# Performance work log

Hardware: AMD Instinct MI355X
Metric: run time of the kernel (lower is better)

## Reference

```python
import jax, jax.numpy as jnp
from jax import lax
import numpy as np

CODE_DIM = 256
CODE_SIZE = 1024
BETA = 0.25


def _conv2d(x, w, b, stride, pad):
    # x: NCHW, w: OIHW (pytorch Conv2d layout)
    y = lax.conv_general_dilated(x, w, (stride, stride), [(pad, pad), (pad, pad)],
                                 dimension_numbers=('NCHW', 'OIHW', 'NCHW'))
    return y + b[None, :, None, None]


def _conv_transpose2d(x, w, b, stride, pad):
    # w: pytorch ConvTranspose2d layout [in, out, kh, kw]
    kh, kw = w.shape[2], w.shape[3]
    wf = jnp.flip(w, (2, 3)).transpose(1, 0, 2, 3)  # -> OIHW with spatial flip
    y = lax.conv_general_dilated(x, wf, (1, 1),
                                 [(kh - 1 - pad, kh - 1 - pad), (kw - 1 - pad, kw - 1 - pad)],
                                 lhs_dilation=(stride, stride),
                                 dimension_numbers=('NCHW', 'OIHW', 'NCHW'))
    return y + b[None, :, None, None]


def setup_inputs() -> dict:
    key = jax.random.key(0)
    ks = jax.random.split(key, 14)
    f32 = jnp.float32

    def p(k, shape, s=0.05):
        return jax.random.normal(k, shape, f32) * s

    return {
        'x': jax.random.normal(ks[0], (64, 1, 128, 128), f32),
        'enc_w1': p(ks[1], (64, 1, 5, 5)), 'enc_b1': jnp.zeros((64,), f32),
        'enc_w2': p(ks[2], (64, 64, 5, 5)), 'enc_b2': jnp.zeros((64,), f32),
        'enc_w3': p(ks[3], (CODE_DIM, 64, 5, 5)), 'enc_b3': jnp.zeros((CODE_DIM,), f32),
        'codebook': p(ks[4], (CODE_SIZE, CODE_DIM)),
        'dec_w1': p(ks[5], (CODE_DIM, 64, 4, 4)), 'dec_b1': jnp.zeros((64,), f32),
        'dec_w2': p(ks[6], (64, 64, 4, 4)), 'dec_b2': jnp.zeros((64,), f32),
        'dec_w3': p(ks[7], (1, 64, 3, 3)), 'dec_b3': jnp.zeros((1,), f32),
    }


def reference(x, enc_w1, enc_b1, enc_w2, enc_b2, enc_w3, enc_b3, codebook,
              dec_w1, dec_b1, dec_w2, dec_b2, dec_w3, dec_b3):
    # ---- encoder ----
    z = jax.nn.relu(_conv2d(x, enc_w1, enc_b1, 2, 2))
    z = jax.nn.relu(_conv2d(z, enc_w2, enc_b2, 1, 2))
    z = _conv2d(z, enc_w3, enc_b3, 2, 2)  # [B, D, H/4, W/4]

    # ---- quantize (eval mode: no EMA buffer updates) ----
    b, c, h, w = z.shape
    flat = z.transpose(0, 2, 3, 1).reshape(-1, c)  # [BHW, D]
    # ||z||^2 - 2 z.W^T + ||w||^2
    dists = ((flat ** 2).sum(axis=1, keepdims=True)
             - 2.0 * flat @ codebook.T
             + (codebook ** 2).sum(axis=1)[None, :])  # [BHW, K]
    idx = jnp.argmin(dists, axis=1)
    e = codebook[idx].reshape(b, h, w, c).transpose(0, 3, 1, 2)  # [B, D, h, w]
    e_st = lax.stop_gradient(e - z) + z  # straight-through

    # ---- decoder ----
    y = jax.nn.relu(_conv_transpose2d(e_st, dec_w1, dec_b1, 2, 1))
    y = jax.nn.relu(_conv_transpose2d(y, dec_w2, dec_b2, 2, 1))
    x_tilde = jnp.tanh(_conv2d(y, dec_w3, dec_b3, 1, 1))

    diff = jnp.mean((z - lax.stop_gradient(e)) ** 2)
    return x_tilde, diff
```

## Files before the change

kernel.cpp:

```cpp
#include <hip/hip_runtime.h>

typedef _Float16 f16;
typedef _Float16 f16x8 __attribute__((ext_vector_type(8)));
typedef _Float16 f16x4 __attribute__((ext_vector_type(4)));
typedef _Float16 h2 __attribute__((ext_vector_type(2)));
typedef float f32x4 __attribute__((ext_vector_type(4)));
typedef unsigned short u16;
typedef unsigned int u32;

#define DEVI __device__ __forceinline__

DEVI u16 f2h(float f) { f16 h = (f16)f; return __builtin_bit_cast(u16, h); }
DEVI float h2f(u16 u) { f16 h = __builtin_bit_cast(f16, u); return (float)h; }

__launch_bounds__(256)
__global__ void prep_wconv_k(const float* __restrict__ src, u16* __restrict__ dst, int nf_sh) {
    int i = blockIdx.x * 256 + threadIdx.x;
    int j = i & 7, lane = (i >> 3) & 63;
    int q = i >> 9;
    int f = q & ((1 << nf_sh) - 1); q >>= nf_sh;
    int pl = q & 1; q >>= 1;
    int icc = q & 1; int tap = q >> 1;
    int oc = (f << 4) + (lane & 15);
    int ic = icc * 32 + ((lane >> 4) << 3) + j;
    float w = src[(oc * 64 + ic) * 25 + tap];
    if (pl == 0) dst[i] = f2h(w);
    else         dst[i] = f2h((w - h2f(f2h(w))) * 4096.f);
}
__launch_bounds__(256)
__global__ void prep_wdec_k(const float* __restrict__ src, u16* __restrict__ dst, int icc_sh) {
    int i = blockIdx.x * 256 + threadIdx.x;
    int j = i & 7, lane = (i >> 3) & 63;
    int f = (i >> 9) & 3;
    int q = i >> 11;
    int icc = q & ((1 << icc_sh) - 1); int tap = q >> icc_sh;
    int oc = (f << 4) + (lane & 15);
    int ic = icc * 32 + ((lane >> 4) << 3) + j;
    dst[i] = f2h(src[(ic * 64 + oc) * 16 + tap]);
}
__launch_bounds__(256)
__global__ void prep_cb_k(const float* __restrict__ cb, u16* __restrict__ dst) {
    int i = blockIdx.x * 256 + threadIdx.x;
    int j = i & 7, lane = (i >> 3) & 63;
    int f = (i >> 9) & 63;
    int q = i >> 15;
    int pl = q & 1; int ks = q >> 1;
    int n = (f << 4) + (lane & 15);
    int k = ks * 32 + ((lane >> 4) << 3) + j;
    float w = cb[n * 256 + k];
    if (pl == 0) dst[i] = f2h(w);
    else         dst[i] = f2h((w - h2f(f2h(w))) * 4096.f);
}
__launch_bounds__(256)
__global__ void prep_cbn_k(const float* __restrict__ cb, float* __restrict__ cbn) {
    int row = blockIdx.x * 256 + threadIdx.x;
    float s = 0.f;
    for (int c = 0; c < 256; c += 4) {
        f32x4 v = *(const f32x4*)&cb[row * 256 + c];
        s = fmaf(v.x, v.x, s); s = fmaf(v.y, v.y, s);
        s = fmaf(v.z, v.z, s); s = fmaf(v.w, v.w, s);
    }
    cbn[row] = s;
}

__launch_bounds__(256)
__global__ void conv1_k(const float* __restrict__ x, const float* __restrict__ w,
                        const float* __restrict__ b, u16* __restrict__ oh, u16* __restrict__ ol) {
    __shared__ float wl[25 * 64];
    __shared__ float bl[64];
    int t = threadIdx.x;
    for (int i = t; i < 1600; i += 256) wl[(i % 25) * 64 + i / 25] = w[i];
    if (t < 64) bl[t] = b[t];
    __syncthreads();
    int p = blockIdx.x * 256 + t;
    int ox = p & 63, oy = (p >> 6) & 63, n = p >> 12;
    f32x4 acc[16];
    #pragma unroll
    for (int c = 0; c < 16; ++c) acc[c] = *(f32x4*)&bl[c * 4];
    for (int dy = 0; dy < 5; ++dy) {
        int iy = 2 * oy - 2 + dy;
        if ((unsigned)iy >= 128u) continue;
        for (int dx = 0; dx < 5; ++dx) {
            int ix = 2 * ox - 2 + dx;
            if ((unsigned)ix >= 128u) continue;
            float v = x[(n * 128 + iy) * 128 + ix];
            const float* wp = &wl[(dy * 5 + dx) * 64];
            #pragma unroll
            for (int c = 0; c < 16; ++c) {
                f32x4 w4 = *(const f32x4*)&wp[c * 4];
                acc[c].x = fmaf(v, w4.x, acc[c].x); acc[c].y = fmaf(v, w4.y, acc[c].y);
                acc[c].z = fmaf(v, w4.z, acc[c].z); acc[c].w = fmaf(v, w4.w, acc[c].w);
            }
        }
    }
    #pragma unroll
    for (int c = 0; c < 16; ++c) {
        ushort4 uh, ul;
        float vv[4] = {acc[c].x, acc[c].y, acc[c].z, acc[c].w};
        u16 rh[4], rl[4];
        #pragma unroll
        for (int k = 0; k < 4; ++k) {
            float v = fmaxf(vv[k], 0.f);
            f16 hh = (f16)v;
            rh[k] = __builtin_bit_cast(u16, hh);
            rl[k] = f2h((v - (float)hh) * 4096.f);
        }
        uh.x = rh[0]; uh.y = rh[1]; uh.z = rh[2]; uh.w = rh[3];
        ul.x = rl[0]; ul.y = rl[1]; ul.z = rl[2]; ul.w = rl[3];
        *(ushort4*)&oh[p * 64 + c * 4] = uh;
        *(ushort4*)&ol[p * 64 + c * 4] = ul;
    }
}

template<int S, int OCT, int NI, bool RELU>
__launch_bounds__(256)
__global__ void conv5_k(const u16* __restrict__ Ah_g, const u16* __restrict__ Al_g,
                        const u16* __restrict__ wBf, const float* __restrict__ bias,
                        u16* __restrict__ Oh, u16* __restrict__ Ol,
                        int IH, int IW, int OH, int OW) {
    constexpr int PATCH = 7 * S + 5;
    constexpr int NPIX = PATCH * PATCH;
    constexpr int NPAIR = (NPIX + 1) / 2;
    constexpr int PLSZ = NPAIR * 64;
    constexpr int NF = OCT / 16;
    constexpr int OCB = OCT / (NI * 64);
    __shared__ u16 patch[2 * PLSZ];

    int t = threadIdx.x, l = t & 63, wv = t >> 6, g = l >> 4;

    int bi = blockIdx.x;
    int wlin = (bi & 7) * ((int)gridDim.x >> 3) + (bi >> 3);
    int ocb = wlin % OCB; int rest = wlin / OCB;
    int tw = OW >> 3, th = OH >> 3;
    int txi = rest % tw; rest /= tw;
    int tyi = rest % th; int n = rest / th;
    int iy0 = S * (tyi << 3) - 2, ix0 = S * (txi << 3) - 2;

    int ppb[4];
    #pragma unroll
    for (int mi = 0; mi < 4; ++mi) {
        int m = mi * 16 + (l & 15);
        ppb[mi] = (S * (m >> 3)) * PATCH + S * (m & 7);
    }

    f32x4 acc0[4][NI], acc1[4][NI];
    f32x4 z4 = {0.f, 0.f, 0.f, 0.f};
    #pragma unroll
    for (int mi = 0; mi < 4; ++mi)
        #pragma unroll
        for (int ni = 0; ni < NI; ++ni) { acc0[mi][ni] = z4; acc1[mi][ni] = z4; }

    int tap0 = bi % 25;
    int dy0 = tap0 / 5, dx0 = tap0 - 5 * dy0;
    int tadd0 = dy0 * PATCH + dx0;
    int iccr = bi & 1;
    int fg = ocb * (4 * NI) + wv * NI;
    const size_t tstride = (size_t)(4 * NF) * 512;

    for (int icci = 0; icci < 2; ++icci) {
        int icc = icci ^ iccr;
        __syncthreads();
        for (int i = t; i < NPIX * 8; i += 256) {
            int c = i & 3; int r2 = i >> 2;
            int pl = (r2 >= NPIX); int pp = r2 - pl * NPIX;
            int py = pp / PATCH, px = pp - py * PATCH;
            int iy = iy0 + py, ix = ix0 + px;
            uint4 v = make_uint4(0u, 0u, 0u, 0u);
            if ((unsigned)iy < (unsigned)IH && (unsigned)ix < (unsigned)IW)
                v = *(const uint4*)&(pl ? Al_g : Ah_g)[(((n * IH + iy) * IW + ix)) * 64 + icc * 32 + c * 8];
            int P = pp >> 1, r = pp & 1;
            *(uint4*)&patch[pl * PLSZ + (P << 6) + (((P + (c << 1) + r) & 7) << 3)] = v;
        }
        __syncthreads();

        const u16* pB = wBf + (size_t)((tap0 * 4 + icc * 2) * NF + fg) * 512 + l * 8;
        int tap = tap0, dx = dx0, tadd = tadd0;
        for (int tapi = 0; tapi < 25; ++tapi) {
            f16x8 Bh[NI], Bl[NI];
            #pragma unroll
            for (int ni = 0; ni < NI; ++ni) {
                Bh[ni] = *(const f16x8*)&pB[ni * 512];
                Bl[ni] = *(const f16x8*)&pB[(NF + ni) * 512];
            }
            f16x8 ah[4], al[4];
            #pragma unroll
            for (int mi = 0; mi < 4; ++mi) {
                int pp = ppb[mi] + tadd;
                int P = pp >> 1, r = pp & 1;
                int offs = (P << 6) + (((P + (g << 1) + r) & 7) << 3);
                ah[mi] = *(const f16x8*)&patch[offs];
                al[mi] = *(const f16x8*)&patch[PLSZ + offs];
            }
            #pragma unroll
            for (int mi = 0; mi < 4; ++mi)
                #pragma unroll
                for (int ni = 0; ni < NI; ++ni) {
                    acc0[mi][ni] = __builtin_amdgcn_mfma_f32_16x16x32_f16(ah[mi], Bh[ni], acc0[mi][ni], 0, 0, 0);
                    acc1[mi][ni] = __builtin_amdgcn_mfma_f32_16x16x32_f16(ah[mi], Bl[ni], acc1[mi][ni], 0, 0, 0);
                    acc1[mi][ni] = __builtin_amdgcn_mfma_f32_16x16x32_f16(al[mi], Bh[ni], acc1[mi][ni], 0, 0, 0);
                }
            pB = (tap == 24) ? (pB - 24 * tstride) : (pB + tstride);
            if (tap == 24) { tap = 0; dx = 0; tadd = 0; }
            else {
                tap++; dx++; tadd++;
                if (dx == 5) { dx = 0; tadd += PATCH - 5; }
            }
        }
    }
    #pragma unroll
    for (int mi = 0; mi < 4; ++mi)
        #pragma unroll
        for (int ni = 0; ni < NI; ++ni) {
            int oc = (fg + ni) * 16 + (l & 15);
            float bv = bias[oc];
            #pragma unroll
            for (int reg = 0; reg < 4; ++reg) {
                float v = acc0[mi][ni][reg] + acc1[mi][ni][reg] * (1.f / 4096.f) + bv;
                if (RELU) v = fmaxf(v, 0.f);
                int pix = mi * 16 + g * 4 + reg;
                int oy = (tyi << 3) + (pix >> 3), ox = (txi << 3) + (pix & 7);
                int idx = ((n * OH + oy) * OW + ox) * OCT + oc;
                f16 hh = (f16)v;
                Oh[idx] = __builtin_bit_cast(u16, hh);
                Ol[idx] = f2h((v - (float)hh) * 4096.f);
            }
        }
}

__launch_bounds__(256, 2)
__global__ void quant_k(const u16* __restrict__ zh, const u16* __restrict__ zl,
                        const u16* __restrict__ cbf, const float* __restrict__ cbn,
                        const float* __restrict__ cb, u16* __restrict__ e,
                        float* __restrict__ diff) {
    __shared__ u16 Bbuf[2 * 32 * 512];
    __shared__ float cbn_l[1024];
    __shared__ float zn_l[128];
    __shared__ float bd_l[128];
    __shared__ int   wi_l[128];

    int t = threadIdx.x, l = t & 63, wv = t >> 6, g = l >> 4;
    int bi = blockIdx.x;
    int row0 = bi << 7;

    {
        f32x4 v = *(const f32x4*)&cbn[t * 4];
        *(f32x4*)&cbn_l[t * 4] = v;
    }

    f16x8 Ah[2][8], Al[2][8];
    int rbase = row0 + wv * 32 + (l & 15);
    #pragma unroll
    for (int mi = 0; mi < 2; ++mi)
        #pragma unroll
        for (int ks = 0; ks < 8; ++ks) {
            size_t off = (size_t)(rbase + mi * 16) * 256 + ks * 32 + g * 8;
            Ah[mi][ks] = *(const f16x8*)&zh[off];
            Al[mi][ks] = *(const f16x8*)&zl[off];
        }

    #pragma unroll
    for (int mi = 0; mi < 2; ++mi) {
        float s = 0.f;
        #pragma unroll
        for (int ks = 0; ks < 8; ++ks)
            #pragma unroll
            for (int j = 0; j < 8; ++j) {
                float v = (float)Ah[mi][ks][j] + (float)Al[mi][ks][j] * (1.f / 4096.f);
                s = fmaf(v, v, s);
            }
        s += __shfl_xor(s, 16);
        s += __shfl_xor(s, 32);
        if (g == 0) zn_l[wv * 32 + mi * 16 + (l & 15)] = s;
    }

    float rd[8]; int rc[8];
    #pragma unroll
    for (int s = 0; s < 8; ++s) { rd[s] = 1e30f; rc[s] = 0; }

    int fi = wv * 8;
    {
        int no0 = bi & 31;
        #pragma unroll
        for (int q = 0; q < 8; ++q) {
            int f2 = fi + q;
            int ks = f2 >> 2, pl = (f2 >> 1) & 1, nf = f2 & 1;
            f16x8 v = *(const f16x8*)&cbf[(size_t)(((ks * 2 + pl) * 64) + no0 * 2 + nf) * 512 + l * 8];
            *(uint4*)&Bbuf[(size_t)f2 * 512 + l * 8] = __builtin_bit_cast(uint4, v);
        }
    }
    __syncthreads();

    for (int noi = 0; noi < 32; ++noi) {
        int b = noi & 1;
        int no_cur = (noi + bi) & 31;

        f16x8 pf[8];
        if (noi < 31) {
            int no_n = (noi + 1 + bi) & 31;
            #pragma unroll
            for (int q = 0; q < 8; ++q) {
                int f2 = fi + q;
                int ks = f2 >> 2, pl = (f2 >> 1) & 1, nf = f2 & 1;
                pf[q] = *(const f16x8*)&cbf[(size_t)(((ks * 2 + pl) * 64) + no_n * 2 + nf) * 512 + l * 8];
            }
        }

        f32x4 acc0[2][2], acc1[2][2];
        f32x4 z4 = {0.f, 0.f, 0.f, 0.f};
        #pragma unroll
        for (int mi = 0; mi < 2; ++mi)
            #pragma unroll
            for (int nf = 0; nf < 2; ++nf) { acc0[mi][nf] = z4; acc1[mi][nf] = z4; }

        #pragma unroll
        for (int ks = 0; ks < 8; ++ks) {
            const u16* bb = &Bbuf[(size_t)(b * 32 + ks * 4) * 512 + l * 8];
            f16x8 Bh0 = *(const f16x8*)&bb[0 * 512];
            f16x8 Bh1 = *(const f16x8*)&bb[1 * 512];
            f16x8 Bl0 = *(const f16x8*)&bb[2 * 512];
            f16x8 Bl1 = *(const f16x8*)&bb[3 * 512];
            #pragma unroll
            for (int mi = 0; mi < 2; ++mi) {
                acc0[mi][0] = __builtin_amdgcn_mfma_f32_16x16x32_f16(Ah[mi][ks], Bh0, acc0[mi][0], 0, 0, 0);
                acc0[mi][1] = __builtin_amdgcn_mfma_f32_16x16x32_f16(Ah[mi][ks], Bh1, acc0[mi][1], 0, 0, 0);
                acc1[mi][0] = __builtin_amdgcn_mfma_f32_16x16x32_f16(Ah[mi][ks], Bl0, acc1[mi][0], 0, 0, 0);
                acc1[mi][0] = __builtin_amdgcn_mfma_f32_16x16x32_f16(Al[mi][ks], Bh0, acc1[mi][0], 0, 0, 0);
                acc1[mi][1] = __builtin_amdgcn_mfma_f32_16x16x32_f16(Ah[mi][ks], Bl1, acc1[mi][1], 0, 0, 0);
                acc1[mi][1] = __builtin_amdgcn_mfma_f32_16x16x32_f16(Al[mi][ks], Bh1, acc1[mi][1], 0, 0, 0);
            }
        }

        #pragma unroll
        for (int nf = 0; nf < 2; ++nf) {
            int col = no_cur * 32 + nf * 16 + (l & 15);
            float cn = cbn_l[col];
            #pragma unroll
            for (int mi = 0; mi < 2; ++mi)
                #pragma unroll
                for (int reg = 0; reg < 4; ++reg) {
                    float d = cn - 2.f * (acc0[mi][nf][reg] + acc1[mi][nf][reg] * (1.f / 4096.f));
                    int slot = mi * 4 + reg;
                    if (d < rd[slot] || (d == rd[slot] && col < rc[slot])) { rd[slot] = d; rc[slot] = col; }
                }
        }

        if (noi < 31) {
            #pragma unroll
            for (int q = 0; q < 8; ++q)
                *(uint4*)&Bbuf[(size_t)((1 - b) * 32 + fi + q) * 512 + l * 8] = __builtin_bit_cast(uint4, pf[q]);
        }
        __syncthreads();
    }

    #pragma unroll
    for (int step = 1; step < 16; step <<= 1) {
        #pragma unroll
        for (int s = 0; s < 8; ++s) {
            float od = __shfl_xor(rd[s], step);
            int ocl = __shfl_xor(rc[s], step);
            if (od < rd[s] || (od == rd[s] && ocl < rc[s])) { rd[s] = od; rc[s] = ocl; }
        }
    }
    if ((l & 15) == 0) {
        #pragma unroll
        for (int s = 0; s < 8; ++s) {
            int mi = s >> 2, reg = s & 3;
            int row = wv * 32 + mi * 16 + g * 4 + reg;
            bd_l[row] = rd[s]; wi_l[row] = rc[s];
        }
    }
    __syncthreads();
    if (t < 64) {
        float dval = (zn_l[t] + bd_l[t]) + (zn_l[t + 64] + bd_l[t + 64]);
        #pragma unroll
        for (int step = 1; step < 64; step <<= 1) dval += __shfl_xor(dval, step);
        if (t == 0) atomicAdd(diff, dval * (1.f / 16777216.f));
    }
    __syncthreads();
    for (int r = 0; r < 128; ++r) {
        int wi = wi_l[r];
        e[(size_t)(row0 + r) * 256 + t] = f2h(cb[wi * 256 + t]);
    }
}

template<int ICT>
__launch_bounds__(256)
__global__ void deconv4_k(const u16* __restrict__ in, const u16* __restrict__ wdf,
                          const float* __restrict__ bias, u16* __restrict__ out,
                          int IH, int IW) {
    constexpr int RST = 40;
    constexpr int ICC = ICT / 32;
    constexpr int PLSZ = 81 * RST;
    __shared__ u16 patch[PLSZ];

    int t = threadIdx.x, l = t & 63, wv = t >> 6;
    int wm = wv >> 1, wn = wv & 1, g = l >> 4;

    int bi = blockIdx.x;
    int wlin = (bi & 7) * ((int)gridDim.x >> 3) + (bi >> 3);
    int par = wlin & 3; int ry = par >> 1, rx = par & 1;
    int rest = wlin >> 2;
    int tw = IW >> 3, th = IH >> 3;
    int txi = rest % tw; rest /= tw;
    int tyi = rest % th; int n = rest / th;
    int a0 = tyi << 3, b0 = txi << 3;
    int by0 = ry ? 0 : -1, bx0 = rx ? 0 : -1;
    int OH = IH << 1, OW = IW << 1;

    int pb0[2];
    #pragma unroll
    for (int mi = 0; mi < 2; ++mi) {
        int m = wm * 32 + mi * 16 + (l & 15);
        int pa = m >> 3, pb_ = m & 7;
        pb0[mi] = (pa * 9 + pb_) * RST + g * 8;
    }

    f32x4 acc[2][2];
    f32x4 z4 = {0.f, 0.f, 0.f, 0.f};
    #pragma unroll
    for (int mi = 0; mi < 2; ++mi)
        #pragma unroll
        for (int ni = 0; ni < 2; ++ni) acc[mi][ni] = z4;

    auto ldB = [&](int icc, int tt, f16x8* B) {
        int tty = tt >> 1, ttx = tt & 1;
        int ky = 1 - ry + 2 * tty, kx = 1 - rx + 2 * ttx;
        int tap = ky * 4 + kx;
        #pragma unroll
        for (int ni = 0; ni < 2; ++ni)
            B[ni] = *(const f16x8*)&wdf[(size_t)((tap * ICC + icc) * 4 + wn * 2 + ni) * 512 + l * 8];
    };

    f16x8 B0[2], B1[2];
    {
        int icc0 = (bi >> 2) & (ICC - 1);
        ldB(icc0, bi & 3, B0);
    }

    for (int icci = 0; icci < ICC; ++icci) {
        int icc = (icci + (bi >> 2)) & (ICC - 1);
        __syncthreads();
        for (int i = t; i < 324; i += 256) {
            int c = i & 3; int pp = i >> 2;
            int pr = pp / 9, pc = pp - pr * 9;
            int ar = a0 + by0 + pr, ac = b0 + bx0 + pc;
            uint4 v = make_uint4(0u, 0u, 0u, 0u);
            if ((unsigned)ar < (unsigned)IH && (unsigned)ac < (unsigned)IW)
                v = *(const uint4*)&in[((n * IH + ar) * IW + ac) * ICT + icc * 32 + c * 8];
            *(uint4*)&patch[(pr * 9 + pc) * RST + c * 8] = v;
        }
        __syncthreads();
        #pragma unroll
        for (int tti = 0; tti < 4; ++tti) {
            int tt = (tti + bi) & 3;
            if (!(icci == ICC - 1 && tti == 3)) {
                int nicci = (tti == 3) ? icci + 1 : icci;
                int ntti = (tti == 3) ? 0 : tti + 1;
                int nicc = (nicci + (bi >> 2)) & (ICC - 1);
                ldB(nicc, (ntti + bi) & 3, B1);
            }
            int tty = tt >> 1, ttx = tt & 1;
            int shift = ((1 - tty) * 9 + (1 - ttx)) * RST;
            #pragma unroll
            for (int mi = 0; mi < 2; ++mi) {
                f16x8 a = *(const f16x8*)&patch[pb0[mi] + shift];
                #pragma unroll
                for (int ni = 0; ni < 2; ++ni)
                    acc[mi][ni] = __builtin_amdgcn_mfma_f32_16x16x32_f16(a, B0[ni], acc[mi][ni], 0, 0, 0);
            }
            B0[0] = B1[0]; B0[1] = B1[1];
        }
    }
    #pragma unroll
    for (int mi = 0; mi < 2; ++mi)
        #pragma unroll
        for (int ni = 0; ni < 2; ++ni) {
            int oc = wn * 32 + ni * 16 + (l & 15);
            float bv = bias[oc];
            #pragma unroll
            for (int reg = 0; reg < 4; ++reg) {
                float v = fmaxf(acc[mi][ni][reg] + bv, 0.f);
                int pix = wm * 32 + mi * 16 + g * 4 + reg;
                int oy = ((a0 + (pix >> 3)) << 1) + ry;
                int ox = ((b0 + (pix & 7)) << 1) + rx;
                out[((n * OH + oy) * OW + ox) * 64 + oc] = f2h(v);
            }
        }
}

__launch_bounds__(256)
__global__ void conv3x3_tanh_k(const u16* __restrict__ in, const float* __restrict__ w,
                               const float* __restrict__ b, float* __restrict__ out) {
    __shared__ u16 tile[18 * 18 * 72];
    __shared__ u32 wpk[288];
    int t = threadIdx.x;
    int bi = blockIdx.x;
    int wlin = (bi & 7) * ((int)gridDim.x >> 3) + (bi >> 3);
    int n = wlin >> 6;
    int tile6 = wlin & 63;
    int ty0 = (tile6 >> 3) << 4, tx0 = (tile6 & 7) << 4;

    for (int i = t; i < 288; i += 256) {
        int tap = i >> 5, icp = i & 31;
        h2 p;
        p.x = (f16)w[(2 * icp) * 9 + tap];
        p.y = (f16)w[(2 * icp + 1) * 9 + tap];
        wpk[tap * 32 + icp] = __builtin_bit_cast(u32, p);
    }
    for (int i = t; i < 2592; i += 256) {
        int ch = i & 7, pix = i >> 3;
        int pr = pix / 18, pc = pix - pr * 18;
        int gy = ty0 - 1 + pr, gx = tx0 - 1 + pc;
        uint4 v = make_uint4(0u, 0u, 0u, 0u);
        if ((unsigned)gy < 128u && (unsigned)gx < 128u)
            v = *(const uint4*)&in[(((n << 7) + gy) * 128 + gx) * 64 + ch * 8];
        *(uint4*)&tile[pix * 72 + ch * 8] = v;
    }
    __syncthreads();

    int ty = t >> 4, tx = t & 15;
    float acc = b[0];
    #pragma unroll
    for (int dy = 0; dy < 3; ++dy) {
        #pragma unroll
        for (int dx = 0; dx < 3; ++dx) {
            int base = ((ty + dy) * 18 + (tx + dx)) * 72;
            const u32* wp = &wpk[(dy * 3 + dx) * 32];
            #pragma unroll
            for (int c8 = 0; c8 < 8; ++c8) {
                uint4 v = *(const uint4*)&tile[base + c8 * 8];
                acc = __builtin_amdgcn_fdot2(__builtin_bit_cast(h2, v.x),
                        __builtin_bit_cast(h2, wp[c8 * 4 + 0]), acc, false);
                acc = __builtin_amdgcn_fdot2(__builtin_bit_cast(h2, v.y),
                        __builtin_bit_cast(h2, wp[c8 * 4 + 1]), acc, false);
                acc = __builtin_amdgcn_fdot2(__builtin_bit_cast(h2, v.z),
                        __builtin_bit_cast(h2, wp[c8 * 4 + 2]), acc, false);
                acc = __builtin_amdgcn_fdot2(__builtin_bit_cast(h2, v.w),
                        __builtin_bit_cast(h2, wp[c8 * 4 + 3]), acc, false);
            }
        }
    }
    int oy = ty0 + ty, ox = tx0 + tx;
    out[(n << 14) + (oy << 7) + ox] = tanhf(acc);
}

extern "C" void kernel_launch(void* const* d_in, const int* in_sizes, int n_in,
                              void* d_out, int out_size, void* d_ws, size_t ws_size,
                              hipStream_t stream) {
    (void)in_sizes; (void)n_in; (void)out_size; (void)ws_size;
    const float* x   = (const float*)d_in[0];
    const float* ew1 = (const float*)d_in[1];
    const float* eb1 = (const float*)d_in[2];
    const float* ew2 = (const float*)d_in[3];
    const float* eb2 = (const float*)d_in[4];
    const float* ew3 = (const float*)d_in[5];
    const float* eb3 = (const float*)d_in[6];
    const float* cb  = (const float*)d_in[7];
    const float* dw1 = (const float*)d_in[8];
    const float* db1 = (const float*)d_in[9];
    const float* dw2 = (const float*)d_in[10];
    const float* db2 = (const float*)d_in[11];
    const float* dw3 = (const float*)d_in[12];
    const float* db3 = (const float*)d_in[13];
    float* out = (float*)d_out;

    u16* ws = (u16*)d_ws;
    u16* a1h = ws;             u16* a1l = ws + 16777216;
    u16* zh  = ws;             u16* zl  = ws + 16777216;
    u16* a2h = ws + 33554432;  u16* a2l = ws + 50331648;
    u16* e   = ws + 33554432;
    u16* y1  = ws + 67108864;
    u16* y2  = ws;
    u16* wBf2 = ws + 83886080;
    u16* wBf3 = wBf2 + 204800;
    u16* wd1f = wBf3 + 819200;
    u16* wd2f = wd1f + 262144;
    u16* cbf  = wd2f + 65536;
    float* cbn = (float*)(cbf + 524288);

    hipMemsetAsync(out + 1048576, 0, 4, stream);

    prep_wconv_k<<<800, 256, 0, stream>>>(ew2, wBf2, 2);
    prep_wconv_k<<<3200, 256, 0, stream>>>(ew3, wBf3, 4);
    prep_wdec_k<<<1024, 256, 0, stream>>>(dw1, wd1f, 3);
    prep_wdec_k<<<256, 256, 0, stream>>>(dw2, wd2f, 1);
    prep_cb_k<<<2048, 256, 0, stream>>>(cb, cbf);
    prep_cbn_k<<<4, 256, 0, stream>>>(cb, cbn);

    conv1_k<<<1024, 256, 0, stream>>>(x, ew1, eb1, a1h, a1l);
    conv5_k<1, 64, 1, true><<<4096, 256, 0, stream>>>(a1h, a1l, wBf2, eb2, a2h, a2l, 64, 64, 64, 64);
    conv5_k<2, 256, 2, false><<<2048, 256, 0, stream>>>(a2h, a2l, wBf3, eb3, zh, zl, 64, 64, 32, 32);
    quant_k<<<512, 256, 0, stream>>>(zh, zl, cbf, cbn, cb, e, out + 1048576);
    deconv4_k<256><<<4096, 256, 0, stream>>>(e, wd1f, db1, y1, 32, 32);
    deconv4_k<64><<<16384, 256, 0, stream>>>(y1, wd2f, db2, y2, 64, 64);
    conv3x3_tanh_k<<<4096, 256, 0, stream>>>(y2, dw3, db3, out);
}
```

Before: 703.2 us.

## Add wider-tile conv5 kernel for second encoder conv with 16x16 output tiles

```diff
diff --git a/kernel.cpp b/kernel.cpp
--- a/kernel.cpp
+++ b/kernel.cpp
@@ -110,6 +110,113 @@
         *(ushort4*)&oh[p * 64 + c * 4] = uh;
         *(ushort4*)&ol[p * 64 + c * 4] = ul;
     }
+}
+
+__launch_bounds__(256, 2)
+__global__ void conv5w_k(const u16* __restrict__ Ah_g, const u16* __restrict__ Al_g,
+                         const u16* __restrict__ wBf, const float* __restrict__ bias,
+                         u16* __restrict__ Oh, u16* __restrict__ Ol) {
+    constexpr int PATCH = 20;
+    constexpr int NPIX = PATCH * PATCH;
+    constexpr int PLSZ = (NPIX / 2) * 64;
+    __shared__ u16 patch[2 * PLSZ];
+
+    int t = threadIdx.x, l = t & 63, wv = t >> 6, g = l >> 4;
+    int qy = wv >> 1, qx = wv & 1;
+
+    int bi = blockIdx.x;
+    int wlin = (bi & 7) * ((int)gridDim.x >> 3) + (bi >> 3);
+    int txi = wlin & 3; int rest = wlin >> 2;
+    int tyi = rest & 3; int n = rest >> 2;
+    int iy0 = (tyi << 4) - 2, ix0 = (txi << 4) - 2;
+
+    int ppb[4];
+    #pragma unroll
+    for (int mi = 0; mi < 4; ++mi) {
+        int m = mi * 16 + (l & 15);
+        ppb[mi] = ((qy << 3) + (m >> 3)) * PATCH + (qx << 3) + (m & 7);
+    }
+
+    f32x4 acc0[4][4], acc1[4][4];
+    f32x4 z4 = {0.f, 0.f, 0.f, 0.f};
+    #pragma unroll
+    for (int mi = 0; mi < 4; ++mi)
+        #pragma unroll
+        for (int ni = 0; ni < 4; ++ni) { acc0[mi][ni] = z4; acc1[mi][ni] = z4; }
+
+    int tap0 = bi % 25;
+    int dy0 = tap0 / 5, dx0 = tap0 - 5 * dy0;
+    int tadd0 = dy0 * PATCH + dx0;
+    int iccr = bi & 1;
+    const size_t tstride = 16 * 512;
+
+    for (int icci = 0; icci < 2; ++icci) {
+        int icc = icci ^ iccr;
+        __syncthreads();
+        for (int i = t; i < NPIX * 8; i += 256) {
+            int c = i & 3; int r2 = i >> 2;
+            int pl = (r2 >= NPIX); int pp = r2 - pl * NPIX;
+            int py = pp / PATCH, px = pp - py * PATCH;
+            int iy = iy0 + py, ix = ix0 + px;
+            uint4 v = make_uint4(0u, 0u, 0u, 0u);
+            if ((unsigned)iy < 64u && (unsigned)ix < 64u)
+                v = *(const uint4*)&(pl ? Al_g : Ah_g)[(((n * 64 + iy) * 64 + ix)) * 64 + icc * 32 + c * 8];
+            int P = pp >> 1, r = pp & 1;
+            int slot = (r << 2) | ((c + P) & 3);
+            *(uint4*)&patch[pl * PLSZ + (P << 6) + (slot << 3)] = v;
+        }
+        __syncthreads();
+
+        const u16* pB = wBf + (size_t)((tap0 * 4 + icc * 2) * 4) * 512 + l * 8;
+        int tap = tap0, dx = dx0, tadd = tadd0;
+        for (int tapi = 0; tapi < 25; ++tapi) {
+            f16x8 Bh[4], Bl[4];
+            #pragma unroll
+            for (int ni = 0; ni < 4; ++ni) {
+                Bh[ni] = *(const f16x8*)&pB[ni * 512];
+                Bl[ni] = *(const f16x8*)&pB[(4 + ni) * 512];
+            }
+            #pragma unroll
+            for (int mi = 0; mi < 4; ++mi) {
+                int pp = ppb[mi] + tadd;
+                int P = pp >> 1, r = pp & 1;
+                int offs = (P << 6) + (((r << 2) | ((g + P) & 3)) << 3);
+                f16x8 ah = *(const f16x8*)&patch[offs];
+                f16x8 al = *(const f16x8*)&patch[PLSZ + offs];
+                #pragma unroll
+                for (int ni = 0; ni < 4; ++ni) {
+                    acc0[mi][ni] = __builtin_amdgcn_mfma_f32_16x16x32_f16(ah, Bh[ni], acc0[mi][ni], 0, 0, 0);
+                    acc1[mi][ni] = __builtin_amdgcn_mfma_f32_16x16x32_f16(ah, Bl[ni], acc1[mi][ni], 0, 0, 0);
+                    acc1[mi][ni] = __builtin_amdgcn_mfma_f32_16x16x32_f16(al, Bh[ni], acc1[mi][ni], 0, 0, 0);
+                }
+            }
+            pB = (tap == 24) ? (pB - 24 * tstride) : (pB + tstride);
+            if (tap == 24) { tap = 0; dx = 0; tadd = 0; }
+            else {
+                tap++; dx++; tadd++;
+                if (dx == 5) { dx = 0; tadd += PATCH - 5; }
+            }
+        }
+    }
+    #pragma unroll
+    for (int mi = 0; mi < 4; ++mi)
+        #pragma unroll
+        for (int ni = 0; ni < 4; ++ni) {
+            int oc = ni * 16 + (l & 15);
+            float bv = bias[oc];
+            #pragma unroll
+            for (int reg = 0; reg < 4; ++reg) {
+                float v = acc0[mi][ni][reg] + acc1[mi][ni][reg] * (1.f / 4096.f) + bv;
+                v = fmaxf(v, 0.f);
+                int pix = mi * 16 + g * 4 + reg;
+                int oy = (tyi << 4) + (qy << 3) + (pix >> 3);
+                int ox = (txi << 4) + (qx << 3) + (pix & 7);
+                int idx = ((n * 64 + oy) * 64 + ox) * 64 + oc;
+                f16 hh = (f16)v;
+                Oh[idx] = __builtin_bit_cast(u16, hh);
+                Ol[idx] = f2h((v - (float)hh) * 4096.f);
+            }
+        }
 }
 
 template<int S, int OCT, int NI, bool RELU>
@@ -588,7 +695,7 @@
     prep_cbn_k<<<4, 256, 0, stream>>>(cb, cbn);
 
     conv1_k<<<1024, 256, 0, stream>>>(x, ew1, eb1, a1h, a1l);
-    conv5_k<1, 64, 1, true><<<4096, 256, 0, stream>>>(a1h, a1l, wBf2, eb2, a2h, a2l, 64, 64, 64, 64);
+    conv5w_k<<<1024, 256, 0, stream>>>(a1h, a1l, wBf2, eb2, a2h, a2l);
     conv5_k<2, 256, 2, false><<<2048, 256, 0, stream>>>(a2h, a2l, wBf3, eb3, zh, zl, 64, 64, 32, 32);
     quant_k<<<512, 256, 0, stream>>>(zh, zl, cbf, cbn, cb, e, out + 1048576);
     deconv4_k<256><<<4096, 256, 0, stream>>>(e, wd1f, db1, y1, 32, 32);
```

Result: faster. 658.1 us (-6.4%).
